# Optimization experiments

Measured on AMD Instinct MI355X. Metric: run time of the kernel, lower is better.

Reference implementation:

```python
import jax, jax.numpy as jnp
import numpy as np
import math

D_MODEL = 512
PATCH_LENS = (8, 16, 32)
MAX_P = 32
TAU = 0.5


def _sinusoid_pe(num_pos, d_model):
    pos = jnp.arange(num_pos, dtype=jnp.float32)[:, None]
    div = jnp.exp(jnp.arange(0, d_model, 2, dtype=jnp.float32) * (-(math.log(10000.0) / d_model)))
    pe = jnp.zeros((num_pos, d_model), dtype=jnp.float32)
    pe = pe.at[:, 0::2].set(jnp.sin(pos * div))
    pe = pe.at[:, 1::2].set(jnp.cos(pos * div))
    return pe  # [num_pos, d_model]


def setup_inputs() -> dict:
    key = jax.random.key(0)
    ks = jax.random.split(key, 10)
    B, C, L = 32, 64, 512
    BC, R, n_exp = B * C, L // MAX_P, len(PATCH_LENS)
    x = jax.random.normal(ks[0], (B, C, L), dtype=jnp.float32)
    u = jax.random.uniform(ks[1], (BC, R, n_exp), dtype=jnp.float32, minval=1e-6, maxval=1.0 - 1e-6)
    gumbel = -jnp.log(-jnp.log(u))
    # router MLP: Linear(max_patch_len, 64) -> ReLU -> Linear(64, n_exp)
    s1 = 1.0 / math.sqrt(MAX_P)
    s2 = 1.0 / math.sqrt(64)
    cls_w1 = jax.random.uniform(ks[2], (MAX_P, 64), jnp.float32, -s1, s1)
    cls_b1 = jax.random.uniform(ks[3], (64,), jnp.float32, -s1, s1)
    cls_w2 = jax.random.uniform(ks[4], (64, n_exp), jnp.float32, -s2, s2)
    cls_b2 = jax.random.uniform(ks[5], (n_exp,), jnp.float32, -s2, s2)
    # per-patch-length expert embeddings: Linear(p, d_model, bias=False)
    emb_w8 = jax.random.uniform(ks[6], (8, D_MODEL), jnp.float32, -1 / math.sqrt(8), 1 / math.sqrt(8))
    emb_w16 = jax.random.uniform(ks[7], (16, D_MODEL), jnp.float32, -1 / math.sqrt(16), 1 / math.sqrt(16))
    emb_w32 = jax.random.uniform(ks[8], (32, D_MODEL), jnp.float32, -1 / math.sqrt(32), 1 / math.sqrt(32))
    return {"x": x, "gumbel": gumbel, "cls_w1": cls_w1, "cls_b1": cls_b1,
            "cls_w2": cls_w2, "cls_b2": cls_b2,
            "emb_w8": emb_w8, "emb_w16": emb_w16, "emb_w32": emb_w32}


def reference(x, gumbel, cls_w1, cls_b1, cls_w2, cls_b2, emb_w8, emb_w16, emb_w32):
    B, C, L = x.shape
    R = L // MAX_P                    # regions per series
    T = MAX_P // min(PATCH_LENS)      # target patches per region (mode='fixed')
    n_exp = len(PATCH_LENS)
    xr = x.reshape(B * C, R, MAX_P)   # [BC, R, P]

    # router MLP per region (vectorized over all regions)
    h = jax.nn.relu(jnp.einsum('brp,pk->brk', xr, cls_w1) + cls_b1)
    logits = jnp.einsum('brk,kn->brn', h, cls_w2) + cls_b2   # [BC, R, n_exp]

    # gumbel-softmax (tau=0.5, hard=True, straight-through)
    y_soft = jax.nn.softmax((logits + gumbel) / TAU, axis=-1)
    idx = jnp.argmax(y_soft, axis=-1)                         # [BC, R]
    y_hard = jax.nn.one_hot(idx, n_exp, dtype=y_soft.dtype)
    cls_soft = y_hard - jax.lax.stop_gradient(y_soft) + y_soft
    cls_pred = jnp.argmax(cls_soft, axis=-1)                  # [BC, R]

    # multi-branch expert embeddings, aligned to T patches via repeat_interleave+truncate
    expert_ws = (emb_w8, emb_w16, emb_w32)
    embs = []
    for p, w in zip(PATCH_LENS, expert_ws):
        n_p = MAX_P // p
        patches = xr.reshape(B * C, R, n_p, p)               # unfold(-1, p, p)
        rep = T - n_p + 1                                     # repeat_interleave factor
        sel = jnp.arange(T) // rep                            # truncated interleave indices
        patches = patches[:, :, sel, :]                       # [BC, R, T, p]
        embs.append(jnp.einsum('brtp,pd->brtd', patches, w))  # [BC, R, T, d]
    stack = jnp.stack(embs, axis=0)                           # [n_exp, BC, R, T, d]

    gates = jnp.transpose(cls_soft, (2, 0, 1))[..., None, None]  # [n_exp, BC, R, 1, 1]
    region_emb = (stack * gates).sum(axis=0)                  # [BC, R, T, d]

    x_patch = region_emb.reshape(B * C, R * T, D_MODEL)
    x_patch = x_patch + _sinusoid_pe(R * T, D_MODEL)[None]

    all_cls_pred = cls_pred.T.reshape(-1)                     # cat over regions along dim 0
    return x_patch, all_cls_pred
```

## Files before the change

kernel.cpp:

```cpp
#include <hip/hip_runtime.h>

#define DM 512
#define BCN 2048
#define XPATCH ((size_t)BCN * 64 * DM)

typedef float f32x8 __attribute__((ext_vector_type(8)));

__device__ __forceinline__ const float* uniform_ptr(const float* p) {
    unsigned long long v = (unsigned long long)p;
    unsigned lo = __builtin_amdgcn_readfirstlane((unsigned)v);
    unsigned hi = __builtin_amdgcn_readfirstlane((unsigned)(v >> 32));
    return (const float*)(((unsigned long long)hi << 32) | lo);
}

__device__ __forceinline__ void sload32(const float* p, f32x8& a, f32x8& b,
                                        f32x8& c, f32x8& d) {
    asm volatile(
        "s_load_dwordx8 %0, %4, 0x0\n\t"
        "s_load_dwordx8 %1, %4, 0x20\n\t"
        "s_load_dwordx8 %2, %4, 0x40\n\t"
        "s_load_dwordx8 %3, %4, 0x60\n\t"
        "s_waitcnt lgkmcnt(0)"
        : "=&s"(a), "=&s"(b), "=&s"(c), "=&s"(d)
        : "s"(uniform_ptr(p)));
}
__device__ __forceinline__ void sload3(const float* p, float& a, float& b, float& c) {
    asm volatile(
        "s_load_dword %0, %3, 0x0\n\t"
        "s_load_dword %1, %3, 0x4\n\t"
        "s_load_dword %2, %3, 0x8\n\t"
        "s_waitcnt lgkmcnt(0)"
        : "=&s"(a), "=&s"(b), "=&s"(c)
        : "s"(uniform_ptr(p)));
}

template<int CTRL>
__device__ __forceinline__ float dpp_add(float x) {
    int mv = __builtin_amdgcn_update_dpp(0, __float_as_int(x), CTRL, 0xf, 0xf, false);
    return x + __int_as_float(mv);
}
__device__ __forceinline__ float wave_sum(float x) {
    x = dpp_add<0x111>(x);
    x = dpp_add<0x112>(x);
    x = dpp_add<0x114>(x);
    x = dpp_add<0x118>(x);
    x = dpp_add<0x142>(x);
    x = dpp_add<0x143>(x);
    return __int_as_float(__builtin_amdgcn_readlane(__float_as_int(x), 63));
}

__global__ __launch_bounds__(512, 4) void ape_fused(
    const float* __restrict__ x,
    const float* __restrict__ gumbel,
    const float* __restrict__ w1,
    const float* __restrict__ b1,
    const float* __restrict__ w2,
    const float* __restrict__ b2,
    const float* __restrict__ w8,
    const float* __restrict__ w16,
    const float* __restrict__ w32,
    float* __restrict__ out)
{
    __shared__ int eidx[2][16];

    const int tid  = threadIdx.x;
    const int lane = tid & 63;
    const int wv   = tid >> 6;
    const int col  = tid;

    float w8r[8], w16r[16], w32r[32], w1r[32];
    #pragma unroll
    for (int q = 0; q < 8;  ++q) w8r[q]  = w8 [(size_t)q * DM + col];
    #pragma unroll
    for (int q = 0; q < 16; ++q) w16r[q] = w16[(size_t)q * DM + col];
    #pragma unroll
    for (int q = 0; q < 32; ++q) w32r[q] = w32[(size_t)q * DM + col];
    #pragma unroll
    for (int q = 0; q < 32; ++q) w1r[q]  = w1[q * 64 + lane];
    const float b1r  = b1[lane];
    const float w2r0 = w2[lane * 3 + 0];
    const float w2r1 = w2[lane * 3 + 1];
    const float w2r2 = w2[lane * 3 + 2];
    const float b20  = b2[0], b21 = b2[1], b22 = b2[2];

    const float kln = -9.210340371976184f / 256.0f;
    const float dv  = __expf(kln * (float)(col >> 1));
    const float ph  = (col & 1) ? 1.5707963267948966f : 0.0f;

    #pragma unroll 1
    for (int i = 0; i < 4; ++i) {
        const int bc = blockIdx.x * 4 + i;
        const float* __restrict__ xrow = x + (size_t)bc * DM;
        int* ei = eidx[i & 1];

        #pragma unroll
        for (int s = 0; s < 2; ++s) {
            const int rr = wv * 2 + s;
            f32x8 xa, xb, xc, xd;
            sload32(xrow + rr * 32, xa, xb, xc, xd);
            float a = b1r;
            #pragma unroll
            for (int q = 0; q < 8; ++q) {
                a = fmaf(xa[q], w1r[q],      a);
                a = fmaf(xb[q], w1r[8 + q],  a);
                a = fmaf(xc[q], w1r[16 + q], a);
                a = fmaf(xd[q], w1r[24 + q], a);
            }
            const float h = fmaxf(a, 0.f);
            float s0 = wave_sum(h * w2r0);
            float s1 = wave_sum(h * w2r1);
            float s2 = wave_sum(h * w2r2);
            float g0, g1, g2;
            sload3(gumbel + ((size_t)bc * 16 + rr) * 3, g0, g1, g2);
            s0 += b20 + g0; s1 += b21 + g1; s2 += b22 + g2;
            int best = 0; float bs = s0;
            if (s1 > bs) { bs = s1; best = 1; }
            if (s2 > bs) best = 2;
            if (lane == 0) {
                ei[rr] = best;
                out[XPATCH + (size_t)rr * BCN + bc] = (float)best;
            }
        }
        __syncthreads();

        #pragma unroll 1
        for (int rr = 0; rr < 16; ++rr) {
            const int e = __builtin_amdgcn_readfirstlane(ei[rr]);
            f32x8 xa, xb, xc, xd;
            sload32(xrow + rr * 32, xa, xb, xc, xd);
            float a0, a1, a2, a3;
            if (e == 0) {
                a0 = a1 = a2 = a3 = 0.f;
                #pragma unroll
                for (int q = 0; q < 8; ++q) {
                    a0 = fmaf(xa[q], w8r[q], a0);
                    a1 = fmaf(xb[q], w8r[q], a1);
                    a2 = fmaf(xc[q], w8r[q], a2);
                    a3 = fmaf(xd[q], w8r[q], a3);
                }
            } else if (e == 1) {
                float d0 = 0.f, d1 = 0.f;
                #pragma unroll
                for (int q = 0; q < 8; ++q) {
                    d0 = fmaf(xa[q], w16r[q],     d0);
                    d0 = fmaf(xb[q], w16r[8 + q], d0);
                    d1 = fmaf(xc[q], w16r[q],     d1);
                    d1 = fmaf(xd[q], w16r[8 + q], d1);
                }
                a0 = a1 = a2 = d0; a3 = d1;
            } else {
                float d = 0.f;
                #pragma unroll
                for (int q = 0; q < 8; ++q) {
                    d = fmaf(xa[q], w32r[q],      d);
                    d = fmaf(xb[q], w32r[8 + q],  d);
                    d = fmaf(xc[q], w32r[16 + q], d);
                    d = fmaf(xd[q], w32r[24 + q], d);
                }
                a0 = a1 = a2 = a3 = d;
            }

            const size_t ob   = ((size_t)(bc * 64 + rr * 4)) * DM + col;
            const float  base = (float)(rr * 4) * dv + ph;
            out[ob]          = a0 + __sinf(base);
            out[ob +     DM] = a1 + __sinf(base + dv);
            out[ob + 2 * DM] = a2 + __sinf(base + 2.f * dv);
            out[ob + 3 * DM] = a3 + __sinf(base + 3.f * dv);
        }
    }
}

extern "C" void kernel_launch(void* const* d_in, const int* in_sizes, int n_in,
                              void* d_out, int out_size, void* d_ws, size_t ws_size,
                              hipStream_t stream) {
    const float* x      = (const float*)d_in[0];
    const float* gumbel = (const float*)d_in[1];
    const float* w1     = (const float*)d_in[2];
    const float* b1     = (const float*)d_in[3];
    const float* w2     = (const float*)d_in[4];
    const float* b2     = (const float*)d_in[5];
    const float* w8     = (const float*)d_in[6];
    const float* w16    = (const float*)d_in[7];
    const float* w32    = (const float*)d_in[8];
    float* out = (float*)d_out;

    ape_fused<<<512, 512, 0, stream>>>(x, gumbel, w1, b1, w2, b2, w8, w16, w32, out);
}
```

Measured before the change: 321.2 us.

## Split columns across blocks, pack expert weights to bf16, and software-pipeline scalar loads

The kernel now launches 2048 blocks of 256 threads, each covering half of the d_model columns for two series instead of all columns for four. Expert weights are packed into bf16 pairs to cut register pressure, with launch bounds raised to 5 blocks per CU. Scalar loads of x and gumbel are issued a step ahead of the compute that uses them, double-buffered, and the gate indices are packed into one register. The bf16 weights lose precision, which risks tolerance failures, and each block now repeats the router classification for its series.

```diff
diff --git a/kernel.cpp b/kernel.cpp
--- a/kernel.cpp
+++ b/kernel.cpp
@@ -1,10 +1,22 @@
 #include <hip/hip_runtime.h>
+#include <hip/hip_bf16.h>
 
 #define DM 512
 #define BCN 2048
 #define XPATCH ((size_t)BCN * 64 * DM)
 
 typedef float f32x8 __attribute__((ext_vector_type(8)));
+
+__device__ __forceinline__ unsigned pack_bf16(float a, float b) {
+    __hip_bfloat162 h = __float22bfloat162_rn(make_float2(a, b));
+    return *reinterpret_cast<unsigned*>(&h);
+}
+__device__ __forceinline__ float2 unpack_bf16(unsigned p) {
+    float2 r;
+    r.x = __uint_as_float(p << 16);
+    r.y = __uint_as_float(p & 0xffff0000u);
+    return r;
+}
 
 __device__ __forceinline__ const float* uniform_ptr(const float* p) {
     unsigned long long v = (unsigned long long)p;
@@ -13,25 +25,27 @@
     return (const float*)(((unsigned long long)hi << 32) | lo);
 }
 
-__device__ __forceinline__ void sload32(const float* p, f32x8& a, f32x8& b,
-                                        f32x8& c, f32x8& d) {
+__device__ __forceinline__ void sload32_issue(const float* p, f32x8& a, f32x8& b,
+                                              f32x8& c, f32x8& d) {
     asm volatile(
         "s_load_dwordx8 %0, %4, 0x0\n\t"
         "s_load_dwordx8 %1, %4, 0x20\n\t"
         "s_load_dwordx8 %2, %4, 0x40\n\t"
-        "s_load_dwordx8 %3, %4, 0x60\n\t"
-        "s_waitcnt lgkmcnt(0)"
+        "s_load_dwordx8 %3, %4, 0x60"
         : "=&s"(a), "=&s"(b), "=&s"(c), "=&s"(d)
         : "s"(uniform_ptr(p)));
 }
-__device__ __forceinline__ void sload3(const float* p, float& a, float& b, float& c) {
+__device__ __forceinline__ void sload3_issue(const float* p, float& a, float& b, float& c) {
     asm volatile(
         "s_load_dword %0, %3, 0x0\n\t"
         "s_load_dword %1, %3, 0x4\n\t"
-        "s_load_dword %2, %3, 0x8\n\t"
-        "s_waitcnt lgkmcnt(0)"
+        "s_load_dword %2, %3, 0x8"
         : "=&s"(a), "=&s"(b), "=&s"(c)
         : "s"(uniform_ptr(p)));
+}
+__device__ __forceinline__ void swait() {
+    asm volatile("s_waitcnt lgkmcnt(0)" ::: "memory");
+    __builtin_amdgcn_sched_barrier(0);
 }
 
 template<int CTRL>
@@ -49,7 +63,17 @@
     return __int_as_float(__builtin_amdgcn_readlane(__float_as_int(x), 63));
 }
 
-__global__ __launch_bounds__(512, 4) void ape_fused(
+__device__ __forceinline__ float dot8p(const f32x8& v, const unsigned* wp, float acc) {
+    #pragma unroll
+    for (int j = 0; j < 4; ++j) {
+        float2 w = unpack_bf16(wp[j]);
+        acc = fmaf(v[2 * j],     w.x, acc);
+        acc = fmaf(v[2 * j + 1], w.y, acc);
+    }
+    return acc;
+}
+
+__global__ __launch_bounds__(256, 5) void ape_fused(
     const float* __restrict__ x,
     const float* __restrict__ gumbel,
     const float* __restrict__ w1,
@@ -66,17 +90,24 @@
     const int tid  = threadIdx.x;
     const int lane = tid & 63;
     const int wv   = tid >> 6;
-    const int col  = tid;
-
-    float w8r[8], w16r[16], w32r[32], w1r[32];
-    #pragma unroll
-    for (int q = 0; q < 8;  ++q) w8r[q]  = w8 [(size_t)q * DM + col];
-    #pragma unroll
-    for (int q = 0; q < 16; ++q) w16r[q] = w16[(size_t)q * DM + col];
-    #pragma unroll
-    for (int q = 0; q < 32; ++q) w32r[q] = w32[(size_t)q * DM + col];
-    #pragma unroll
-    for (int q = 0; q < 32; ++q) w1r[q]  = w1[q * 64 + lane];
+    const int hf   = blockIdx.x & 1;
+    const int bc0  = (blockIdx.x >> 1) * 2;
+    const int col  = tid + (hf << 8);
+
+    unsigned w8p[4], w16p[8], w32p[16];
+    #pragma unroll
+    for (int j = 0; j < 4; ++j)
+        w8p[j]  = pack_bf16(w8 [(size_t)(2*j) * DM + col], w8 [(size_t)(2*j+1) * DM + col]);
+    #pragma unroll
+    for (int j = 0; j < 8; ++j)
+        w16p[j] = pack_bf16(w16[(size_t)(2*j) * DM + col], w16[(size_t)(2*j+1) * DM + col]);
+    #pragma unroll
+    for (int j = 0; j < 16; ++j)
+        w32p[j] = pack_bf16(w32[(size_t)(2*j) * DM + col], w32[(size_t)(2*j+1) * DM + col]);
+
+    float w1r[32];
+    #pragma unroll
+    for (int q = 0; q < 32; ++q) w1r[q] = w1[q * 64 + lane];
     const float b1r  = b1[lane];
     const float w2r0 = w2[lane * 3 + 0];
     const float w2r1 = w2[lane * 3 + 1];
@@ -88,84 +119,111 @@
     const float ph  = (col & 1) ? 1.5707963267948966f : 0.0f;
 
     #pragma unroll 1
-    for (int i = 0; i < 4; ++i) {
-        const int bc = blockIdx.x * 4 + i;
+    for (int i = 0; i < 2; ++i) {
+        const int bc = bc0 + i;
         const float* __restrict__ xrow = x + (size_t)bc * DM;
-        int* ei = eidx[i & 1];
-
-        #pragma unroll
-        for (int s = 0; s < 2; ++s) {
-            const int rr = wv * 2 + s;
-            f32x8 xa, xb, xc, xd;
-            sload32(xrow + rr * 32, xa, xb, xc, xd);
+        int* ei = eidx[i];
+
+        auto classify = [&](int rr, const f32x8& va, const f32x8& vb,
+                            const f32x8& vc, const f32x8& vd,
+                            float g0, float g1, float g2) {
             float a = b1r;
             #pragma unroll
             for (int q = 0; q < 8; ++q) {
-                a = fmaf(xa[q], w1r[q],      a);
-                a = fmaf(xb[q], w1r[8 + q],  a);
-                a = fmaf(xc[q], w1r[16 + q], a);
-                a = fmaf(xd[q], w1r[24 + q], a);
+                a = fmaf(va[q], w1r[q],      a);
+                a = fmaf(vb[q], w1r[8 + q],  a);
+                a = fmaf(vc[q], w1r[16 + q], a);
+                a = fmaf(vd[q], w1r[24 + q], a);
             }
             const float h = fmaxf(a, 0.f);
-            float s0 = wave_sum(h * w2r0);
-            float s1 = wave_sum(h * w2r1);
-            float s2 = wave_sum(h * w2r2);
-            float g0, g1, g2;
-            sload3(gumbel + ((size_t)bc * 16 + rr) * 3, g0, g1, g2);
-            s0 += b20 + g0; s1 += b21 + g1; s2 += b22 + g2;
+            float s0 = wave_sum(h * w2r0) + b20 + g0;
+            float s1 = wave_sum(h * w2r1) + b21 + g1;
+            float s2 = wave_sum(h * w2r2) + b22 + g2;
             int best = 0; float bs = s0;
             if (s1 > bs) { bs = s1; best = 1; }
             if (s2 > bs) best = 2;
             if (lane == 0) {
                 ei[rr] = best;
-                out[XPATCH + (size_t)rr * BCN + bc] = (float)best;
-            }
+                if (hf == 0)
+                    out[XPATCH + (size_t)rr * BCN + bc] = (float)best;
+            }
+        };
+
+        {
+            const int r0 = wv * 4;
+            const float* gb = gumbel + ((size_t)bc * 16 + r0) * 3;
+            f32x8 pa, pb, pc, pd, qa, qb, qc, qd;
+            float pg0, pg1, pg2, qg0, qg1, qg2;
+            sload32_issue(xrow + r0 * 32, pa, pb, pc, pd);
+            sload3_issue(gb, pg0, pg1, pg2);
+
+            swait();
+            sload32_issue(xrow + (r0 + 1) * 32, qa, qb, qc, qd);
+            sload3_issue(gb + 3, qg0, qg1, qg2);
+            classify(r0 + 0, pa, pb, pc, pd, pg0, pg1, pg2);
+
+            swait();
+            sload32_issue(xrow + (r0 + 2) * 32, pa, pb, pc, pd);
+            sload3_issue(gb + 6, pg0, pg1, pg2);
+            classify(r0 + 1, qa, qb, qc, qd, qg0, qg1, qg2);
+
+            swait();
+            sload32_issue(xrow + (r0 + 3) * 32, qa, qb, qc, qd);
+            sload3_issue(gb + 9, qg0, qg1, qg2);
+            classify(r0 + 2, pa, pb, pc, pd, pg0, pg1, pg2);
+
+            swait();
+            classify(r0 + 3, qa, qb, qc, qd, qg0, qg1, qg2);
         }
         __syncthreads();
 
-        #pragma unroll 1
-        for (int rr = 0; rr < 16; ++rr) {
-            const int e = __builtin_amdgcn_readfirstlane(ei[rr]);
-            f32x8 xa, xb, xc, xd;
-            sload32(xrow + rr * 32, xa, xb, xc, xd);
+        unsigned ep = 0;
+        #pragma unroll
+        for (int r = 0; r < 16; ++r) ep |= ((unsigned)(ei[r] & 3)) << (2 * r);
+        ep = (unsigned)__builtin_amdgcn_readfirstlane((int)ep);
+
+        auto regB = [&](int rr, const f32x8& va, const f32x8& vb,
+                        const f32x8& vc, const f32x8& vd) {
+            const int e = (int)((ep >> (2 * rr)) & 3u);
             float a0, a1, a2, a3;
             if (e == 0) {
-                a0 = a1 = a2 = a3 = 0.f;
-                #pragma unroll
-                for (int q = 0; q < 8; ++q) {
-                    a0 = fmaf(xa[q], w8r[q], a0);
-                    a1 = fmaf(xb[q], w8r[q], a1);
-                    a2 = fmaf(xc[q], w8r[q], a2);
-                    a3 = fmaf(xd[q], w8r[q], a3);
-                }
+                a0 = dot8p(va, w8p, 0.f);
+                a1 = dot8p(vb, w8p, 0.f);
+                a2 = dot8p(vc, w8p, 0.f);
+                a3 = dot8p(vd, w8p, 0.f);
             } else if (e == 1) {
-                float d0 = 0.f, d1 = 0.f;
-                #pragma unroll
-                for (int q = 0; q < 8; ++q) {
-                    d0 = fmaf(xa[q], w16r[q],     d0);
-                    d0 = fmaf(xb[q], w16r[8 + q], d0);
-                    d1 = fmaf(xc[q], w16r[q],     d1);
-                    d1 = fmaf(xd[q], w16r[8 + q], d1);
-                }
+                float d0 = dot8p(vb, w16p + 4, dot8p(va, w16p, 0.f));
+                float d1 = dot8p(vd, w16p + 4, dot8p(vc, w16p, 0.f));
                 a0 = a1 = a2 = d0; a3 = d1;
             } else {
-                float d = 0.f;
-                #pragma unroll
-                for (int q = 0; q < 8; ++q) {
-                    d = fmaf(xa[q], w32r[q],      d);
-                    d = fmaf(xb[q], w32r[8 + q],  d);
-                    d = fmaf(xc[q], w32r[16 + q], d);
-                    d = fmaf(xd[q], w32r[24 + q], d);
-                }
+                float d = dot8p(vd, w32p + 12,
+                          dot8p(vc, w32p + 8,
+                          dot8p(vb, w32p + 4,
+                          dot8p(va, w32p, 0.f))));
                 a0 = a1 = a2 = a3 = d;
             }
-
             const size_t ob   = ((size_t)(bc * 64 + rr * 4)) * DM + col;
             const float  base = (float)(rr * 4) * dv + ph;
             out[ob]          = a0 + __sinf(base);
             out[ob +     DM] = a1 + __sinf(base + dv);
             out[ob + 2 * DM] = a2 + __sinf(base + 2.f * dv);
             out[ob + 3 * DM] = a3 + __sinf(base + 3.f * dv);
+        };
+
+        {
+            f32x8 Aa, Ab, Ac, Ad, Ba, Bb, Bc, Bd;
+            sload32_issue(xrow, Aa, Ab, Ac, Ad);
+            #pragma unroll 1
+            for (int r2 = 0; r2 < 8; ++r2) {
+                const int ra = r2 * 2;
+                swait();
+                sload32_issue(xrow + (ra + 1) * 32, Ba, Bb, Bc, Bd);
+                regB(ra, Aa, Ab, Ac, Ad);
+                swait();
+                if (r2 < 7)
+                    sload32_issue(xrow + (ra + 2) * 32, Aa, Ab, Ac, Ad);
+                regB(ra + 1, Ba, Bb, Bc, Bd);
+            }
         }
     }
 }
@@ -184,5 +242,5 @@
     const float* w32    = (const float*)d_in[8];
     float* out = (float*)d_out;
 
-    ape_fused<<<512, 512, 0, stream>>>(x, gumbel, w1, b1, w2, b2, w8, w16, w32, out);
-}
+    ape_fused<<<2048, 256, 0, stream>>>(x, gumbel, w1, b1, w2, b2, w8, w16, w32, out);
+}
```

New measurement: 503.1 us. +56.6%, slower.
